# Performance work log

Measured on AMD Instinct MI355X. Metric: run time of the kernel, lower is better.

The kernel has to match this reference:

```python
import jax, jax.numpy as jnp
import numpy as np

HEADS = 4
W1 = 7
W2 = 5

def _ln_channel(x, g, b):
    # x: [B,C,H,W]; LayerNorm over channel dim (permute to channel-last)
    xt = x.transpose(0, 2, 3, 1)
    mu = xt.mean(-1, keepdims=True)
    var = xt.var(-1, keepdims=True)
    xt = (xt - mu) / jnp.sqrt(var + 1e-5) * g + b
    return xt.transpose(0, 3, 1, 2)

def _neighborhood_attention(x, qkv_w, qkv_b, proj_w, proj_b, rpb, heads, w):
    # x: [B,C,H,W]; clamped sliding-window (NAT) attention with rel-pos bias
    B, C, H, Wd = x.shape
    hd = C // heads
    xl = x.transpose(0, 2, 3, 1)                      # [B,H,W,C]
    qkv = xl @ qkv_w.T + qkv_b                        # [B,H,W,3C]
    qkv = qkv.reshape(B, H, Wd, 3, heads, hd)
    q = qkv[:, :, :, 0].transpose(0, 3, 1, 2, 4)      # [B,h,H,W,d]
    k = qkv[:, :, :, 1].transpose(0, 3, 1, 2, 4)
    v = qkv[:, :, :, 2].transpose(0, 3, 1, 2, 4)
    q = q * (hd ** -0.5)
    # clamped neighborhood start per row/col
    si = jnp.clip(jnp.arange(H) - w // 2, 0, H - w)   # [H]
    sj = jnp.clip(jnp.arange(Wd) - w // 2, 0, Wd - w) # [W]
    idx_i = si[:, None] + jnp.arange(w)[None, :]      # [H,w]
    idx_j = sj[:, None] + jnp.arange(w)[None, :]      # [W,w]
    # gather neighbor keys/values: [B,h,H,W,w,w,d]
    k_nb = k[:, :, idx_i[:, None, :, None], idx_j[None, :, None, :], :]
    v_nb = v[:, :, idx_i[:, None, :, None], idx_j[None, :, None, :], :]
    attn = jnp.einsum('bnijd,bnijkld->bnijkl', q, k_nb)  # [B,h,H,W,w,w]
    # relative position bias: rel = (w-1) + neighbor_offset - query_offset
    pi = jnp.arange(H) - si                            # [H] in [0,w-1]
    pj = jnp.arange(Wd) - sj
    bi = (w - 1) + jnp.arange(w)[None, :] - pi[:, None]  # [H,w]
    bj = (w - 1) + jnp.arange(w)[None, :] - pj[:, None]  # [W,w]
    bias = rpb[:, bi[:, None, :, None], bj[None, :, None, :]]  # [h,H,W,w,w]
    attn = attn + bias[None]
    attn = jax.nn.softmax(attn.reshape(B, heads, H, Wd, w * w), axis=-1)
    attn = attn.reshape(B, heads, H, Wd, w, w)
    out = jnp.einsum('bnijkl,bnijkld->bnijd', attn, v_nb)  # [B,h,H,W,d]
    out = out.transpose(0, 2, 3, 1, 4).reshape(B, H, Wd, C)
    out = out @ proj_w.T + proj_b
    return out.transpose(0, 3, 1, 2)                   # [B,C,H,W]

def setup_inputs() -> dict:
    key = jax.random.key(0)
    ks = jax.random.split(key, 12)
    B, C, H, W = 2, 128, 56, 56
    s = 0.02
    return {
        'x': jax.random.normal(ks[0], (B, C, H, W), jnp.float32),
        'ln1_g': jnp.ones((C,), jnp.float32),
        'ln1_b': jnp.zeros((C,), jnp.float32),
        'qkv_w1': jax.random.normal(ks[1], (3 * C, C), jnp.float32) * s,
        'qkv_b1': jnp.zeros((3 * C,), jnp.float32),
        'proj_w1': jax.random.normal(ks[2], (C, C), jnp.float32) * s,
        'proj_b1': jnp.zeros((C,), jnp.float32),
        'rpb1': jax.random.normal(ks[3], (HEADS, 2 * W1 - 1, 2 * W1 - 1), jnp.float32) * s,
        'qkv_w2': jax.random.normal(ks[4], (3 * C, C), jnp.float32) * s,
        'qkv_b2': jnp.zeros((3 * C,), jnp.float32),
        'proj_w2': jax.random.normal(ks[5], (C, C), jnp.float32) * s,
        'proj_b2': jnp.zeros((C,), jnp.float32),
        'rpb2': jax.random.normal(ks[6], (HEADS, 2 * W2 - 1, 2 * W2 - 1), jnp.float32) * s,
        'ln2_g': jnp.ones((C,), jnp.float32),
        'ln2_b': jnp.zeros((C,), jnp.float32),
        'fc1_w': jax.random.normal(ks[7], (2 * C, C), jnp.float32) * s,
        'fc1_b': jnp.zeros((2 * C,), jnp.float32),
        'fc2_w': jax.random.normal(ks[8], (C, 2 * C), jnp.float32) * s,
        'fc2_b': jnp.zeros((C,), jnp.float32),
    }

def reference(x, ln1_g, ln1_b, qkv_w1, qkv_b1, proj_w1, proj_b1, rpb1,
              qkv_w2, qkv_b2, proj_w2, proj_b2, rpb2,
              ln2_g, ln2_b, fc1_w, fc1_b, fc2_w, fc2_b):
    xn = _ln_channel(x, ln1_g, ln1_b)
    a = (_neighborhood_attention(xn, qkv_w1, qkv_b1, proj_w1, proj_b1, rpb1, HEADS, W1)
         + _neighborhood_attention(xn, qkv_w2, qkv_b2, proj_w2, proj_b2, rpb2, HEADS, W2))
    x = x + a
    xn2 = _ln_channel(x, ln2_g, ln2_b)
    h = jnp.einsum('bchw,oc->bohw', xn2, fc1_w) + fc1_b[None, :, None, None]
    h = jax.nn.gelu(h, approximate=False)  # torch nn.GELU default = exact erf
    y = jnp.einsum('bchw,oc->bohw', h, fc2_w) + fc2_b[None, :, None, None]
    return x + y
```

## Files before the change

kernel.cpp:

```cpp
#include <hip/hip_runtime.h>
#include <hip/hip_bf16.h>

#define BATCH 2
#define CH    128
#define HH    56
#define WW    56
#define HWS   3136
#define NPOS  6272
#define HEADS 4
#define HD    32

using f32x4 = __attribute__((ext_vector_type(4))) float;
using s16x8 = __attribute__((ext_vector_type(8))) short;

__device__ __forceinline__ unsigned short f2bf(float f) {
  unsigned u = __builtin_bit_cast(unsigned, f);
  u += 0x7FFFu + ((u >> 16) & 1u);
  return (unsigned short)(u >> 16);
}
__device__ __forceinline__ unsigned pack2bf(float a, float b) {
  return (unsigned)f2bf(a) | ((unsigned)f2bf(b) << 16);
}
__device__ __forceinline__ float4 bf4tof(uint2 u) {
  float4 r;
  r.x = __builtin_bit_cast(float, u.x << 16);
  r.y = __builtin_bit_cast(float, u.x & 0xFFFF0000u);
  r.z = __builtin_bit_cast(float, u.y << 16);
  r.w = __builtin_bit_cast(float, u.y & 0xFFFF0000u);
  return r;
}

__global__ __launch_bounds__(256) void ln1_kernel(const float* __restrict__ x,
                                                  const float* __restrict__ g,
                                                  const float* __restrict__ be,
                                                  unsigned short* __restrict__ out) {
  __shared__ float tile[128 * 65];
  __shared__ float mu_s[64];
  __shared__ float rs_s[64];
  const int p0 = blockIdx.x * 64;
  const int b  = (p0 >= HWS) ? 1 : 0;
  const int s0 = p0 - b * HWS;
  const int tid = threadIdx.x;

  for (int idx = tid; idx < 8192; idx += 256) {
    int c = idx >> 6, p = idx & 63;
    tile[c * 65 + p] = x[(size_t)(b * CH + c) * HWS + s0 + p];
  }
  __syncthreads();
  {
    int p = tid >> 2, q = tid & 3;
    float sum = 0.f, sq = 0.f;
#pragma unroll
    for (int t = 0; t < 32; ++t) {
      float v = tile[(q * 32 + t) * 65 + p];
      sum += v; sq += v * v;
    }
    sum += __shfl_xor(sum, 1); sq += __shfl_xor(sq, 1);
    sum += __shfl_xor(sum, 2); sq += __shfl_xor(sq, 2);
    float mu  = sum * 0.0078125f;
    float var = sq * 0.0078125f - mu * mu;
    float rs  = rsqrtf(var + 1e-5f);
    if (q == 0) { mu_s[p] = mu; rs_s[p] = rs; }
  }
  __syncthreads();
  for (int idx = tid; idx < 4096; idx += 256) {
    int nl = idx >> 6, c2 = idx & 63;
    int c0 = 2 * c2;
    float v0 = (tile[c0 * 65 + nl] - mu_s[nl]) * rs_s[nl] * g[c0] + be[c0];
    float v1 = (tile[(c0 + 1) * 65 + nl] - mu_s[nl]) * rs_s[nl] * g[c0 + 1] + be[c0 + 1];
    reinterpret_cast<unsigned*>(out)[(size_t)(p0 + nl) * 64 + c2] = pack2bf(v0, v1);
  }
}

__device__ __forceinline__ void stage_tile(const unsigned short* __restrict__ src,
                                           int stride, int row0, int kElems,
                                           int tid, char* dstB) {
  const int upr = kElems >> 3;
  const int total = 64 * upr;
#pragma unroll
  for (int u = tid; u < total; u += 256) {
    int row = u / upr;
    int ku  = u % upr;
    int byte = row * (kElems << 1) + (ku << 4);
    byte ^= (row & 7) << 4;
    *reinterpret_cast<uint4*>(dstB + byte) =
        *reinterpret_cast<const uint4*>(src + (size_t)(row0 + row) * stride + (ku << 3));
  }
}

__device__ __forceinline__ void stage_tile_f32(const float* __restrict__ src,
                                               int stride, int row0, int kElems,
                                               int tid, char* dstB) {
  const int upr = kElems >> 3;
  const int total = 64 * upr;
#pragma unroll
  for (int u = tid; u < total; u += 256) {
    int row = u / upr;
    int ku  = u % upr;
    int byte = row * (kElems << 1) + (ku << 4);
    byte ^= (row & 7) << 4;
    const float* s = src + (size_t)(row0 + row) * stride + (ku << 3);
    float4 va = *reinterpret_cast<const float4*>(s);
    float4 vb = *reinterpret_cast<const float4*>(s + 4);
    uint4 o;
    o.x = pack2bf(va.x, va.y);
    o.y = pack2bf(va.z, va.w);
    o.z = pack2bf(vb.x, vb.y);
    o.w = pack2bf(vb.z, vb.w);
    *reinterpret_cast<uint4*>(dstB + byte) = o;
  }
}

__device__ __forceinline__ void tile_compute2(const char* AsB, int aStrideB, int aKoffB,
                                              const char* WsB, int wStrideB, int wKoffB,
                                              int lane, int wr, int wc,
                                              f32x4 (&acc)[2][2]) {
  const int r_lo = lane & 15, kg = lane >> 4;
#pragma unroll
  for (int ks = 0; ks < 2; ++ks) {
    const int ko = ks * 64 + kg * 16;
    const int koffA = aKoffB + ko;
    const int koffW = wKoffB + ko;
    s16x8 a[2], bf[2];
#pragma unroll
    for (int fi = 0; fi < 2; ++fi) {
      int row = wr * 32 + fi * 16 + r_lo;
      int byte = row * aStrideB + koffA; byte ^= (row & 7) << 4;
      a[fi] = *reinterpret_cast<const s16x8*>(AsB + byte);
    }
#pragma unroll
    for (int ci = 0; ci < 2; ++ci) {
      int row = wc * 32 + ci * 16 + r_lo;
      int byte = row * wStrideB + koffW; byte ^= (row & 7) << 4;
      bf[ci] = *reinterpret_cast<const s16x8*>(WsB + byte);
    }
#pragma unroll
    for (int fi = 0; fi < 2; ++fi)
#pragma unroll
      for (int ci = 0; ci < 2; ++ci)
        acc[fi][ci] = __builtin_amdgcn_mfma_f32_16x16x32_bf16(a[fi], bf[ci], acc[fi][ci], 0, 0, 0);
  }
}

__device__ __forceinline__ float gelu_exact(float v) {
  return 0.5f * v * (1.0f + erff(v * 0.70710678118654752f));
}

__global__ __launch_bounds__(256) void qkv_mfma(const unsigned short* __restrict__ A,
                                                const float* __restrict__ W1f,
                                                const float* __restrict__ b1,
                                                unsigned short* __restrict__ o1,
                                                const float* __restrict__ W2f,
                                                const float* __restrict__ b2,
                                                unsigned short* __restrict__ o2) {
  __shared__ char AsB[16384];
  __shared__ char WsB[16384];
  const int tid = threadIdx.x;
  const int lane = tid & 63, w = tid >> 6, wr = w >> 1, wc = w & 1;
  const int p0 = blockIdx.x * 64;
  const int yy = blockIdx.y;
  const bool first = yy < 6;
  const float* Wf = first ? W1f : W2f;
  const float* bias = first ? b1 : b2;
  unsigned short* outp = first ? o1 : o2;
  const int n0 = (first ? yy : yy - 6) * 64;

  stage_tile(A, 128, p0, 128, tid, AsB);
  stage_tile_f32(Wf, 128, n0, 128, tid, WsB);

  f32x4 acc[2][2];
#pragma unroll
  for (int i = 0; i < 2; ++i)
#pragma unroll
    for (int j = 0; j < 2; ++j) acc[i][j] = (f32x4){0.f, 0.f, 0.f, 0.f};

  __syncthreads();
  tile_compute2(AsB, 256, 0,   WsB, 256, 0,   lane, wr, wc, acc);
  tile_compute2(AsB, 256, 128, WsB, 256, 128, lane, wr, wc, acc);

  const int r_lo = lane & 15, kg = lane >> 4;
#pragma unroll
  for (int ci = 0; ci < 2; ++ci) {
    int col = n0 + wc * 32 + ci * 16 + r_lo;
    float bc = bias[col];
#pragma unroll
    for (int fi = 0; fi < 2; ++fi) {
      int row0 = p0 + wr * 32 + fi * 16 + kg * 4;
#pragma unroll
      for (int r = 0; r < 4; ++r)
        outp[(size_t)(row0 + r) * 384 + col] = f2bf(acc[fi][ci][r] + bc);
    }
  }
}

__global__ __launch_bounds__(256) void proj_mfma(const unsigned short* __restrict__ A1,
                                                 const float* __restrict__ W1f,
                                                 const float* __restrict__ b1,
                                                 const unsigned short* __restrict__ A2,
                                                 const float* __restrict__ W2f,
                                                 const float* __restrict__ b2,
                                                 const float* __restrict__ xres,
                                                 float* __restrict__ x2out) {
  __shared__ char A1B[16384];
  __shared__ char W1B[16384];
  __shared__ char A2B[16384];
  __shared__ char W2B[16384];
  const int tid = threadIdx.x;
  const int lane = tid & 63, w = tid >> 6, wr = w >> 1, wc = w & 1;
  const int p0 = blockIdx.x * 64, n0 = blockIdx.y * 64;
  const int bb = (p0 >= HWS) ? 1 : 0;
  const int s0 = p0 - bb * HWS;

  stage_tile(A1, 128, p0, 128, tid, A1B);
  stage_tile_f32(W1f, 128, n0, 128, tid, W1B);
  stage_tile(A2, 128, p0, 128, tid, A2B);
  stage_tile_f32(W2f, 128, n0, 128, tid, W2B);

  f32x4 acc[2][2];
#pragma unroll
  for (int i = 0; i < 2; ++i)
#pragma unroll
    for (int j = 0; j < 2; ++j) acc[i][j] = (f32x4){0.f, 0.f, 0.f, 0.f};

  __syncthreads();
  tile_compute2(A1B, 256, 0,   W1B, 256, 0,   lane, wr, wc, acc);
  tile_compute2(A1B, 256, 128, W1B, 256, 128, lane, wr, wc, acc);
  tile_compute2(A2B, 256, 0,   W2B, 256, 0,   lane, wr, wc, acc);
  tile_compute2(A2B, 256, 128, W2B, 256, 128, lane, wr, wc, acc);

  const int r_lo = lane & 15, kg = lane >> 4;
#pragma unroll
  for (int ci = 0; ci < 2; ++ci) {
    int col = n0 + wc * 32 + ci * 16 + r_lo;
    float bc = b1[col] + b2[col];
#pragma unroll
    for (int fi = 0; fi < 2; ++fi) {
      int rloc = wr * 32 + fi * 16 + kg * 4;
      float4 xr = *reinterpret_cast<const float4*>(
          &xres[(size_t)(bb * CH + col) * HWS + s0 + rloc]);
      int row0 = p0 + rloc;
      x2out[(size_t)(row0 + 0) * CH + col] = acc[fi][ci][0] + bc + xr.x;
      x2out[(size_t)(row0 + 1) * CH + col] = acc[fi][ci][1] + bc + xr.y;
      x2out[(size_t)(row0 + 2) * CH + col] = acc[fi][ci][2] + bc + xr.z;
      x2out[(size_t)(row0 + 3) * CH + col] = acc[fi][ci][3] + bc + xr.w;
    }
  }
}

__global__ __launch_bounds__(256) void fc1ln_mfma(const float* __restrict__ x2,
                                                  const float* __restrict__ g,
                                                  const float* __restrict__ be,
                                                  const float* __restrict__ Wf,
                                                  const float* __restrict__ bias,
                                                  unsigned short* __restrict__ out) {
  __shared__ char AsB[16384];
  __shared__ char WsB[16384];
  const int tid = threadIdx.x;
  const int lane = tid & 63, w = tid >> 6, wr = w >> 1, wc = w & 1;
  const int p0 = blockIdx.x * 64, n0 = blockIdx.y * 64;
  {
    const int p = tid >> 2, q = tid & 3;
    const float* row = x2 + (size_t)(p0 + p) * CH + q * 32;
    float4 v[8];
    float sum = 0.f, sq = 0.f;
#pragma unroll
    for (int t = 0; t < 8; ++t) {
      v[t] = *reinterpret_cast<const float4*>(row + t * 4);
      sum += v[t].x + v[t].y + v[t].z + v[t].w;
      sq  += v[t].x * v[t].x + v[t].y * v[t].y + v[t].z * v[t].z + v[t].w * v[t].w;
    }
    sum += __shfl_xor(sum, 1); sq += __shfl_xor(sq, 1);
    sum += __shfl_xor(sum, 2); sq += __shfl_xor(sq, 2);
    float mu = sum * 0.0078125f;
    float rs = rsqrtf(sq * 0.0078125f - mu * mu + 1e-5f);
#pragma unroll
    for (int t = 0; t < 8; t += 2) {
      int d0 = q * 32 + t * 4;
      float4 g0 = *reinterpret_cast<const float4*>(g + d0);
      float4 g1 = *reinterpret_cast<const float4*>(g + d0 + 4);
      float4 b0 = *reinterpret_cast<const float4*>(be + d0);
      float4 b1v = *reinterpret_cast<const float4*>(be + d0 + 4);
      uint4 o;
      o.x = pack2bf((v[t].x - mu) * rs * g0.x + b0.x, (v[t].y - mu) * rs * g0.y + b0.y);
      o.y = pack2bf((v[t].z - mu) * rs * g0.z + b0.z, (v[t].w - mu) * rs * g0.w + b0.w);
      o.z = pack2bf((v[t+1].x - mu) * rs * g1.x + b1v.x, (v[t+1].y - mu) * rs * g1.y + b1v.y);
      o.w = pack2bf((v[t+1].z - mu) * rs * g1.z + b1v.z, (v[t+1].w - mu) * rs * g1.w + b1v.w);
      int byte = p * 256 + q * 64 + (t >> 1) * 16;
      byte ^= (p & 7) << 4;
      *reinterpret_cast<uint4*>(AsB + byte) = o;
    }
  }
  stage_tile_f32(Wf, 128, n0, 128, tid, WsB);

  f32x4 acc[2][2];
#pragma unroll
  for (int i = 0; i < 2; ++i)
#pragma unroll
    for (int j = 0; j < 2; ++j) acc[i][j] = (f32x4){0.f, 0.f, 0.f, 0.f};

  __syncthreads();
  tile_compute2(AsB, 256, 0,   WsB, 256, 0,   lane, wr, wc, acc);
  tile_compute2(AsB, 256, 128, WsB, 256, 128, lane, wr, wc, acc);

  const int r_lo = lane & 15, kg = lane >> 4;
#pragma unroll
  for (int ci = 0; ci < 2; ++ci) {
    int col = n0 + wc * 32 + ci * 16 + r_lo;
    float bc = bias[col];
#pragma unroll
    for (int fi = 0; fi < 2; ++fi) {
      int row0 = p0 + wr * 32 + fi * 16 + kg * 4;
#pragma unroll
      for (int r = 0; r < 4; ++r)
        out[(size_t)(row0 + r) * 256 + col] = f2bf(gelu_exact(acc[fi][ci][r] + bc));
    }
  }
}

__global__ __launch_bounds__(256) void fc2_mfma(const unsigned short* __restrict__ A,
                                                const float* __restrict__ Wf,
                                                const float* __restrict__ bias,
                                                const float* __restrict__ x2,
                                                float* __restrict__ out) {
  __shared__ char AsB[32768];
  __shared__ char WsB[32768];
  const int tid = threadIdx.x;
  const int lane = tid & 63, w = tid >> 6, wr = w >> 1, wc = w & 1;
  const int p0 = blockIdx.x * 64, n0 = blockIdx.y * 64;
  const int bb = (p0 >= HWS) ? 1 : 0;
  const int s0 = p0 - bb * HWS;

  stage_tile(A, 256, p0, 256, tid, AsB);
  stage_tile_f32(Wf, 256, n0, 256, tid, WsB);

  f32x4 acc[2][2];
#pragma unroll
  for (int i = 0; i < 2; ++i)
#pragma unroll
    for (int j = 0; j < 2; ++j) acc[i][j] = (f32x4){0.f, 0.f, 0.f, 0.f};

  __syncthreads();
#pragma unroll
  for (int kb = 0; kb < 4; ++kb)
    tile_compute2(AsB, 512, kb * 128, WsB, 512, kb * 128, lane, wr, wc, acc);

  const int r_lo = lane & 15, kg = lane >> 4;
#pragma unroll
  for (int ci = 0; ci < 2; ++ci) {
    int col = n0 + wc * 32 + ci * 16 + r_lo;
    float bc = bias[col];
#pragma unroll
    for (int fi = 0; fi < 2; ++fi) {
      int rloc = wr * 32 + fi * 16 + kg * 4;
      int row0 = p0 + rloc;
      float4 o;
      o.x = acc[fi][ci][0] + bc + x2[(size_t)(row0 + 0) * CH + col];
      o.y = acc[fi][ci][1] + bc + x2[(size_t)(row0 + 1) * CH + col];
      o.z = acc[fi][ci][2] + bc + x2[(size_t)(row0 + 2) * CH + col];
      o.w = acc[fi][ci][3] + bc + x2[(size_t)(row0 + 3) * CH + col];
      *reinterpret_cast<float4*>(&out[(size_t)(bb * CH + col) * HWS + s0 + rloc]) = o;
    }
  }
}

template <int NW>
__device__ __forceinline__ void natten_body(const unsigned short* __restrict__ qkvb,
                                            const float* __restrict__ rpb,
                                            unsigned short* __restrict__ out,
                                            int blk, int tid) {
  const int g   = blk * 32 + (tid >> 3);
  const int sub = tid & 7;
  const int j  = g % WW;
  const int t1 = g / WW;
  const int i  = t1 % HH;
  const int t2 = t1 / HH;
  const int h  = t2 & 3;
  const int b  = t2 >> 2;
  const int n  = b * HWS + i * WW + j;

  const float scale = 0.17677669529663687f;
  float4 q = bf4tof(*reinterpret_cast<const uint2*>(qkvb + (size_t)n * 384 + h * 32 + sub * 4));
  q.x *= scale; q.y *= scale; q.z *= scale; q.w *= scale;

  const int si = min(max(i - NW / 2, 0), HH - NW);
  const int sj = min(max(j - NW / 2, 0), WW - NW);
  const float* rb = rpb + h * (2 * NW - 1) * (2 * NW - 1)
                    + (NW - 1 - (i - si)) * (2 * NW - 1) + (NW - 1 - (j - sj));
  float sc[NW * NW];
  float mx = -1e30f;
#pragma unroll
  for (int ki = 0; ki < NW; ++ki) {
#pragma unroll
    for (int kj = 0; kj < NW; ++kj) {
      const int nn = b * HWS + (si + ki) * WW + sj + kj;
      float4 k4 = bf4tof(*reinterpret_cast<const uint2*>(
          qkvb + (size_t)nn * 384 + 128 + h * 32 + sub * 4));
      float p = q.x * k4.x + q.y * k4.y + q.z * k4.z + q.w * k4.w;
      p += __shfl_xor(p, 1);
      p += __shfl_xor(p, 2);
      p += __shfl_xor(p, 4);
      p += rb[ki * (2 * NW - 1) + kj];
      sc[ki * NW + kj] = p;
      mx = fmaxf(mx, p);
    }
  }
  float ssum = 0.f;
#pragma unroll
  for (int kk = 0; kk < NW * NW; ++kk) {
    sc[kk] = __expf(sc[kk] - mx);
    ssum += sc[kk];
  }
  float4 o = make_float4(0.f, 0.f, 0.f, 0.f);
#pragma unroll
  for (int ki = 0; ki < NW; ++ki) {
#pragma unroll
    for (int kj = 0; kj < NW; ++kj) {
      const int nn = b * HWS + (si + ki) * WW + sj + kj;
      float4 v4 = bf4tof(*reinterpret_cast<const uint2*>(
          qkvb + (size_t)nn * 384 + 256 + h * 32 + sub * 4));
      float p = sc[ki * NW + kj];
      o.x = fmaf(p, v4.x, o.x);
      o.y = fmaf(p, v4.y, o.y);
      o.z = fmaf(p, v4.z, o.z);
      o.w = fmaf(p, v4.w, o.w);
    }
  }
  float inv = 1.0f / ssum;
  uint2 ov;
  ov.x = pack2bf(o.x * inv, o.y * inv);
  ov.y = pack2bf(o.z * inv, o.w * inv);
  *reinterpret_cast<uint2*>(out + (size_t)n * CH + h * 32 + sub * 4) = ov;
}

__global__ __launch_bounds__(256) void natten_fused(const unsigned short* __restrict__ qkv1,
                                                    const float* __restrict__ rpb1,
                                                    unsigned short* __restrict__ a1,
                                                    const unsigned short* __restrict__ qkv2,
                                                    const float* __restrict__ rpb2,
                                                    unsigned short* __restrict__ a2) {
  if (blockIdx.x < 784) natten_body<7>(qkv1, rpb1, a1, blockIdx.x, threadIdx.x);
  else                  natten_body<5>(qkv2, rpb2, a2, blockIdx.x - 784, threadIdx.x);
}

extern "C" void kernel_launch(void* const* d_in, const int* in_sizes, int n_in,
                              void* d_out, int out_size, void* d_ws, size_t ws_size,
                              hipStream_t stream) {
  const float* x       = (const float*)d_in[0];
  const float* ln1_g   = (const float*)d_in[1];
  const float* ln1_b   = (const float*)d_in[2];
  const float* qkv_w1  = (const float*)d_in[3];
  const float* qkv_b1  = (const float*)d_in[4];
  const float* proj_w1 = (const float*)d_in[5];
  const float* proj_b1 = (const float*)d_in[6];
  const float* rpb1    = (const float*)d_in[7];
  const float* qkv_w2  = (const float*)d_in[8];
  const float* qkv_b2  = (const float*)d_in[9];
  const float* proj_w2 = (const float*)d_in[10];
  const float* proj_b2 = (const float*)d_in[11];
  const float* rpb2    = (const float*)d_in[12];
  const float* ln2_g   = (const float*)d_in[13];
  const float* ln2_b   = (const float*)d_in[14];
  const float* fc1_w   = (const float*)d_in[15];
  const float* fc1_b   = (const float*)d_in[16];
  const float* fc2_w   = (const float*)d_in[17];
  const float* fc2_b   = (const float*)d_in[18];
  float* out = (float*)d_out;

  char* wsb = (char*)d_ws;
  unsigned short* xn    = (unsigned short*)(wsb);
  unsigned short* qkv1  = (unsigned short*)(wsb + 1605632);
  unsigned short* qkv2  = (unsigned short*)(wsb + 6422528);
  unsigned short* attn1 = (unsigned short*)(wsb + 11239424);
  unsigned short* attn2 = (unsigned short*)(wsb + 12845056);
  float*          x2    = (float*)(wsb + 14450688);
  unsigned short* hbuf  = (unsigned short*)(wsb + 17661952);

  ln1_kernel<<<98, 256, 0, stream>>>(x, ln1_g, ln1_b, xn);
  qkv_mfma<<<dim3(98, 12), 256, 0, stream>>>(xn, qkv_w1, qkv_b1, qkv1,
                                             qkv_w2, qkv_b2, qkv2);
  natten_fused<<<1568, 256, 0, stream>>>(qkv1, rpb1, attn1, qkv2, rpb2, attn2);
  proj_mfma<<<dim3(98, 2), 256, 0, stream>>>(attn1, proj_w1, proj_b1,
                                             attn2, proj_w2, proj_b2, x, x2);
  fc1ln_mfma<<<dim3(98, 4), 256, 0, stream>>>(x2, ln2_g, ln2_b, fc1_w, fc1_b, hbuf);
  fc2_mfma<<<dim3(98, 2), 256, 0, stream>>>(hbuf, fc2_w, fc2_b, x2, out);
}
```

Baseline: 158.4 us.

## Use single-pass online softmax in NATTEN and interleave block mapping across heads

Replaces the three-pass neighborhood attention (scores, exp/sum, weighted V) with a single online-softmax pass that reads K and V in the same loop. It rescales lazily, only when the running max grows by more than 8, which removes the per-thread score array and its register pressure. Row base pointers are hoisted out of the inner loop. Block indices are also swizzled so that consecutive workgroups alternate between the 7x7 and 5x5 attention bodies, balancing work across compute units at the cost of some locality.

```diff
diff --git a/kernel.cpp b/kernel.cpp
--- a/kernel.cpp
+++ b/kernel.cpp
@@ -386,46 +386,35 @@
   const int sj = min(max(j - NW / 2, 0), WW - NW);
   const float* rb = rpb + h * (2 * NW - 1) * (2 * NW - 1)
                     + (NW - 1 - (i - si)) * (2 * NW - 1) + (NW - 1 - (j - sj));
-  float sc[NW * NW];
-  float mx = -1e30f;
+  float m = -1e30f, l = 0.f;
+  float4 o = make_float4(0.f, 0.f, 0.f, 0.f);
 #pragma unroll
   for (int ki = 0; ki < NW; ++ki) {
+    const unsigned short* rowp =
+        qkvb + (size_t)(b * HWS + (si + ki) * WW + sj) * 384 + 128 + h * 32 + sub * 4;
 #pragma unroll
     for (int kj = 0; kj < NW; ++kj) {
-      const int nn = b * HWS + (si + ki) * WW + sj + kj;
-      float4 k4 = bf4tof(*reinterpret_cast<const uint2*>(
-          qkvb + (size_t)nn * 384 + 128 + h * 32 + sub * 4));
+      float4 k4 = bf4tof(*reinterpret_cast<const uint2*>(rowp + kj * 384));
       float p = q.x * k4.x + q.y * k4.y + q.z * k4.z + q.w * k4.w;
       p += __shfl_xor(p, 1);
       p += __shfl_xor(p, 2);
       p += __shfl_xor(p, 4);
       p += rb[ki * (2 * NW - 1) + kj];
-      sc[ki * NW + kj] = p;
-      mx = fmaxf(mx, p);
-    }
-  }
-  float ssum = 0.f;
-#pragma unroll
-  for (int kk = 0; kk < NW * NW; ++kk) {
-    sc[kk] = __expf(sc[kk] - mx);
-    ssum += sc[kk];
-  }
-  float4 o = make_float4(0.f, 0.f, 0.f, 0.f);
-#pragma unroll
-  for (int ki = 0; ki < NW; ++ki) {
-#pragma unroll
-    for (int kj = 0; kj < NW; ++kj) {
-      const int nn = b * HWS + (si + ki) * WW + sj + kj;
-      float4 v4 = bf4tof(*reinterpret_cast<const uint2*>(
-          qkvb + (size_t)nn * 384 + 256 + h * 32 + sub * 4));
-      float p = sc[ki * NW + kj];
-      o.x = fmaf(p, v4.x, o.x);
-      o.y = fmaf(p, v4.y, o.y);
-      o.z = fmaf(p, v4.z, o.z);
-      o.w = fmaf(p, v4.w, o.w);
-    }
-  }
-  float inv = 1.0f / ssum;
+      if (p > m + 8.f) {
+        float r = __expf(m - p);
+        l *= r; o.x *= r; o.y *= r; o.z *= r; o.w *= r;
+        m = p;
+      }
+      float e = __expf(p - m);
+      l += e;
+      float4 v4 = bf4tof(*reinterpret_cast<const uint2*>(rowp + kj * 384 + 128));
+      o.x = fmaf(e, v4.x, o.x);
+      o.y = fmaf(e, v4.y, o.y);
+      o.z = fmaf(e, v4.z, o.z);
+      o.w = fmaf(e, v4.w, o.w);
+    }
+  }
+  float inv = 1.0f / l;
   uint2 ov;
   ov.x = pack2bf(o.x * inv, o.y * inv);
   ov.y = pack2bf(o.z * inv, o.w * inv);
@@ -438,8 +427,9 @@
                                                     const unsigned short* __restrict__ qkv2,
                                                     const float* __restrict__ rpb2,
                                                     unsigned short* __restrict__ a2) {
-  if (blockIdx.x < 784) natten_body<7>(qkv1, rpb1, a1, blockIdx.x, threadIdx.x);
-  else                  natten_body<5>(qkv2, rpb2, a2, blockIdx.x - 784, threadIdx.x);
+  const int swz = (blockIdx.x & 7) * 196 + (blockIdx.x >> 3);
+  if (swz < 784) natten_body<7>(qkv1, rpb1, a1, swz, threadIdx.x);
+  else           natten_body<5>(qkv2, rpb2, a2, swz - 784, threadIdx.x);
 }
 
 extern "C" void kernel_launch(void* const* d_in, const int* in_sizes, int n_in,
```

New measurement: 157.3 us. No clear change (-0.7%).
